# Performance work log

Measured on AMD Instinct MI355X. Metric: run time of the kernel, lower is better.

The kernel has to match this reference:

```python
import jax, jax.numpy as jnp
import numpy as np

NUM_ENTITIES = 100000
NUM_RELATIONS = 500
DIM = 256
NUM_TRIANGLES = 300000
NUM_TETRAS = 150000
ET_EDGES = 900000   # ~3 entities per triangle
TT_EDGES = 600000   # ~4 triangles per tetra
ENT_TET_EDGES = 600000
BATCH = 8192


def _mean_aggregate(src_idx, dst_idx, src, num_dst):
    """Scatter-mean of src[src_idx] into num_dst buckets keyed by dst_idx."""
    agg = jax.ops.segment_sum(src[src_idx], dst_idx, num_segments=num_dst)
    cnt = jax.ops.segment_sum(jnp.ones_like(dst_idx, dtype=src.dtype), dst_idx,
                              num_segments=num_dst)
    return agg / jnp.maximum(cnt, 1.0)[:, None]


def setup_inputs() -> dict:
    key = jax.random.key(0)
    ks = jax.random.split(key, 16)
    s = 1.0 / np.sqrt(DIM)
    E = jax.random.normal(ks[0], (NUM_ENTITIES, DIM), jnp.float32) * s
    R = jax.random.normal(ks[1], (NUM_RELATIONS, DIM), jnp.float32) * s
    lin2_w = jax.random.normal(ks[2], (DIM, DIM), jnp.float32) * s
    lin2_b = jnp.zeros((DIM,), jnp.float32)
    lin3_w = jax.random.normal(ks[3], (DIM, DIM), jnp.float32) * s
    lin3_b = jnp.zeros((DIM,), jnp.float32)
    t2e_w = jax.random.normal(ks[4], (DIM, DIM), jnp.float32) * s
    t2e_b = jnp.zeros((DIM,), jnp.float32)
    fusion_alpha = jnp.zeros((2,), jnp.float32)
    gamma = jnp.array([12.0], jnp.float32)
    # bipartite edge lists: row 0 = src indices, row 1 = dst indices
    et = jnp.stack([
        jax.random.randint(ks[5], (ET_EDGES,), 0, NUM_ENTITIES),
        jax.random.randint(ks[6], (ET_EDGES,), 0, NUM_TRIANGLES)], axis=0)
    tt = jnp.stack([
        jax.random.randint(ks[7], (TT_EDGES,), 0, NUM_TRIANGLES),
        jax.random.randint(ks[8], (TT_EDGES,), 0, NUM_TETRAS)], axis=0)
    # entity_tetra_index: row 0 = entity, row 1 = tetra (flipped inside model)
    etet = jnp.stack([
        jax.random.randint(ks[9], (ENT_TET_EDGES,), 0, NUM_ENTITIES),
        jax.random.randint(ks[10], (ENT_TET_EDGES,), 0, NUM_TETRAS)], axis=0)
    triples = jnp.stack([
        jax.random.randint(ks[11], (BATCH,), 0, NUM_ENTITIES),
        jax.random.randint(ks[12], (BATCH,), 0, NUM_RELATIONS),
        jax.random.randint(ks[13], (BATCH,), 0, NUM_ENTITIES)], axis=1)
    return {"E": E, "R": R, "lin2_w": lin2_w, "lin2_b": lin2_b,
            "lin3_w": lin3_w, "lin3_b": lin3_b, "t2e_w": t2e_w, "t2e_b": t2e_b,
            "fusion_alpha": fusion_alpha, "gamma": gamma,
            "entity_triangle_index": et, "triangle_tetra_index": tt,
            "entity_tetra_index": etet, "triples": triples,
            "num_triangles": NUM_TRIANGLES, "num_tetras": NUM_TETRAS}


def reference(E, R, lin2_w, lin2_b, lin3_w, lin3_b, t2e_w, t2e_b,
              fusion_alpha, gamma, entity_triangle_index, triangle_tetra_index,
              entity_tetra_index, triples, num_triangles, num_tetras):
    # gnn2: entity -> triangle (scatter-mean + Linear + ReLU)
    tri_agg = _mean_aggregate(entity_triangle_index[0], entity_triangle_index[1],
                              E, num_triangles)                      # [T, d]
    tri_emb = jax.nn.relu(tri_agg @ lin2_w.T + lin2_b)
    # gnn3: triangle -> tetra
    tet_agg = _mean_aggregate(triangle_tetra_index[0], triangle_tetra_index[1],
                              tri_emb, num_tetras)                   # [K, d]
    tet_emb = jax.nn.relu(tet_agg @ lin3_w.T + lin3_b)
    tet_proj = tet_emb @ t2e_w.T + t2e_b                             # [K, d]
    # tetra -> entity (edge index flipped: src=tetra, dst=entity)
    v_topo = _mean_aggregate(entity_tetra_index[1], entity_tetra_index[0],
                             tet_proj, E.shape[0])                   # [N, d]
    # learned fusion
    w = jax.nn.softmax(fusion_alpha)
    V = w[0] * E + w[1] * v_topo
    # TransE scoring: gamma - ||V[h] + R[r] - V[t]||
    h, r, t = triples[:, 0], triples[:, 1], triples[:, 2]
    diff = V[h] + R[r] - V[t]
    return gamma[0] - jnp.sqrt(jnp.sum(diff * diff, axis=-1))
```

## Files before the change

### kernel.cpp

```cpp
#include <hip/hip_runtime.h>
#include <hip/hip_bf16.h>
#include <math.h>

#define DIM 256
#define SBS 256
#define SIT 16
#define NT   300000
#define NTET 150000

typedef __attribute__((ext_vector_type(8))) short          bf16x8;
typedef __attribute__((ext_vector_type(8))) unsigned short u16x8;
typedef __attribute__((ext_vector_type(4))) float          f32x4;

__device__ inline float b2f(unsigned short u) {
    union { unsigned int i; float f; } c; c.i = ((unsigned int)u) << 16; return c.f;
}
__device__ inline unsigned short f2b(float f) {
    __hip_bfloat16 h = __float2bfloat16(f);
    return *reinterpret_cast<unsigned short*>(&h);
}
__device__ inline bool bmget(const unsigned* bm, int i) {
    return (bm[i >> 5] >> (i & 31)) & 1u;
}

__global__ __launch_bounds__(256) void k_cast3(
    const float* __restrict__ w2, const float* __restrict__ w3,
    const float* __restrict__ wt, unsigned short* __restrict__ out)
{
    int i = (blockIdx.x * 256 + threadIdx.x) * 4;
    const float* src; int l;
    if (i < 65536)       { src = w2; l = i; }
    else if (i < 131072) { src = w3; l = i - 65536; }
    else                 { src = wt; l = i - 131072; }
    float4 v = *(const float4*)(src + l);
    ushort4 o; o.x = f2b(v.x); o.y = f2b(v.y); o.z = f2b(v.z); o.w = f2b(v.w);
    *(ushort4*)(out + i) = o;
}

__global__ __launch_bounds__(256) void k_mark(
    const int* __restrict__ trip, unsigned* __restrict__ bm, int B)
{
    int i = blockIdx.x * 256 + threadIdx.x;
    if (i < 2 * B) {
        int ent = trip[(i >> 1) * 3 + ((i & 1) ? 2 : 0)];
        atomicOr(&bm[ent >> 5], 1u << (ent & 31));
    }
}

__global__ __launch_bounds__(256) void k_markf(
    const int* __restrict__ mi, const int* __restrict__ ci,
    const unsigned* __restrict__ bmIn, unsigned* __restrict__ bmOut, int n)
{
    int e = blockIdx.x * 256 + threadIdx.x;
    if (e < n && bmget(bmIn, ci[e])) {
        int m = mi[e];
        atomicOr(&bmOut[m >> 5], 1u << (m & 31));
    }
}

__global__ __launch_bounds__(256) void k_count_all(
    const int* __restrict__ et, const int* __restrict__ tt, const int* __restrict__ etet,
    const unsigned* __restrict__ bmTri, const unsigned* __restrict__ bmTet,
    const unsigned* __restrict__ bmEnt, int* __restrict__ cnt,
    int ET, int TT, int ETET)
{
    int e = blockIdx.x * 256 + threadIdx.x;
    if (e < ET) {
        int d = et[ET + e];
        if (bmget(bmTri, d)) atomicAdd(&cnt[d], 1);
    } else if (e < ET + TT) {
        int i = e - ET;
        int d = tt[TT + i];
        if (bmget(bmTet, d)) atomicAdd(&cnt[NT + d], 1);
    } else if (e < ET + TT + ETET) {
        int i = e - ET - TT;
        int d = etet[i];
        if (bmget(bmEnt, d)) atomicAdd(&cnt[NT + NTET + d], 1);
    }
}

__global__ __launch_bounds__(SBS) void k_scan_block(
    const int* __restrict__ cnt, int* __restrict__ rowOff,
    int* __restrict__ blockSums, int n)
{
    __shared__ int lds[SBS];
    const int t = threadIdx.x;
    const int tbase = blockIdx.x * SBS * SIT + t * SIT;
    int v[SIT]; int tsum = 0;
    #pragma unroll
    for (int i = 0; i < SIT; ++i) {
        int idx = tbase + i;
        v[i] = (idx < n) ? cnt[idx] : 0;
        tsum += v[i];
    }
    lds[t] = tsum;
    __syncthreads();
    #pragma unroll
    for (int off = 1; off < SBS; off <<= 1) {
        int y = (t >= off) ? lds[t - off] : 0;
        __syncthreads();
        lds[t] += y;
        __syncthreads();
    }
    int incl = lds[t];
    int run = incl - tsum;
    #pragma unroll
    for (int i = 0; i < SIT; ++i) {
        int idx = tbase + i;
        if (idx < n) rowOff[idx] = run;
        run += v[i];
    }
    if (t == SBS - 1) blockSums[blockIdx.x] = incl;
}

__global__ __launch_bounds__(SBS) void k_scan_sums(int* __restrict__ bs, int nb)
{
    __shared__ int lds[SBS];
    const int t = threadIdx.x;
    int v = (t < nb) ? bs[t] : 0;
    lds[t] = v;
    __syncthreads();
    #pragma unroll
    for (int off = 1; off < SBS; off <<= 1) {
        int y = (t >= off) ? lds[t - off] : 0;
        __syncthreads();
        lds[t] += y;
        __syncthreads();
    }
    if (t < nb) {
        bs[t] = lds[t] - v;
        if (t == nb - 1) bs[nb] = lds[t];
    }
}

__global__ __launch_bounds__(256) void k_scan_add(
    int* __restrict__ rowOff, int* __restrict__ cursor,
    const int* __restrict__ bs, int n, int nb)
{
    int i = blockIdx.x * 256 + threadIdx.x;
    if (i < n) {
        int v = rowOff[i] + bs[i / (SBS * SIT)];
        rowOff[i] = v;
        cursor[i] = v;
    }
    if (i == 0) rowOff[n] = bs[nb];
}

__global__ __launch_bounds__(256) void k_place_all(
    const int* __restrict__ et, const int* __restrict__ tt, const int* __restrict__ etet,
    const unsigned* __restrict__ bmTri, const unsigned* __restrict__ bmTet,
    const unsigned* __restrict__ bmEnt, int* __restrict__ cursor,
    int* __restrict__ sorted, int ET, int TT, int ETET)
{
    int e = blockIdx.x * 256 + threadIdx.x;
    if (e < ET) {
        int d = et[ET + e];
        if (bmget(bmTri, d)) sorted[atomicAdd(&cursor[d], 1)] = et[e];
    } else if (e < ET + TT) {
        int i = e - ET;
        int d = tt[TT + i];
        if (bmget(bmTet, d)) sorted[atomicAdd(&cursor[NT + d], 1)] = tt[i];
    } else if (e < ET + TT + ETET) {
        int i = e - ET - TT;
        int d = etet[i];
        if (bmget(bmEnt, d)) sorted[atomicAdd(&cursor[NT + NTET + d], 1)] = etet[ETET + i];
    }
}

template<int EPI>
__global__ __launch_bounds__(256) void k_gather(
    const unsigned short* __restrict__ src, const int* __restrict__ sorted,
    const int* __restrict__ rowOff, const float* __restrict__ bias,
    const float* __restrict__ E, const float* __restrict__ alpha,
    const unsigned* __restrict__ bm, void* __restrict__ out, int ndst)
{
    int d    = (blockIdx.x * 256 + threadIdx.x) >> 6;
    int lane = threadIdx.x & 63;
    if (d >= ndst) return;
    if (!bmget(bm, d)) return;
    int e0 = rowOff[d], e1 = rowOff[d + 1];
    float ax = 0.f, ay = 0.f, az = 0.f, aw = 0.f;
    int base = e0;
    for (; base + 4 <= e1; base += 4) {
        #pragma unroll
        for (int j = 0; j < 4; ++j) {
            int s = sorted[base + j];
            ushort4 u = *(const ushort4*)(src + (size_t)s * DIM + lane * 4);
            ax += b2f(u.x); ay += b2f(u.y); az += b2f(u.z); aw += b2f(u.w);
        }
    }
    if (base < e1) {
        #pragma unroll
        for (int j = 0; j < 4; ++j) {
            int ee = base + j;
            int ec = (ee < e1) ? ee : (e1 - 1);
            int s  = sorted[ec];
            ushort4 u = *(const ushort4*)(src + (size_t)s * DIM + lane * 4);
            float g = (ee < e1) ? 1.0f : 0.0f;
            ax += g * b2f(u.x); ay += g * b2f(u.y);
            az += g * b2f(u.z); aw += g * b2f(u.w);
        }
    }
    float inv = 1.0f / fmaxf((float)(e1 - e0), 1.0f);
    ax *= inv; ay *= inv; az *= inv; aw *= inv;
    if (EPI == 0) {
        float4 bv = *(const float4*)(bias + lane * 4);
        ax = fmaxf(ax + bv.x, 0.f); ay = fmaxf(ay + bv.y, 0.f);
        az = fmaxf(az + bv.z, 0.f); aw = fmaxf(aw + bv.w, 0.f);
        ushort4 o; o.x = f2b(ax); o.y = f2b(ay); o.z = f2b(az); o.w = f2b(aw);
        *(ushort4*)((unsigned short*)out + (size_t)d * DIM + lane * 4) = o;
    } else if (EPI == 1) {
        ushort4 o; o.x = f2b(ax); o.y = f2b(ay); o.z = f2b(az); o.w = f2b(aw);
        *(ushort4*)((unsigned short*)out + (size_t)d * DIM + lane * 4) = o;
    } else {
        float a0 = alpha[0], a1 = alpha[1];
        float mx = fmaxf(a0, a1);
        float x0 = expf(a0 - mx), x1 = expf(a1 - mx);
        float w0 = x0 / (x0 + x1), w1 = x1 / (x0 + x1);
        float4 ev = *(const float4*)(E + (size_t)d * DIM + lane * 4);
        float4 o;
        o.x = w0 * ev.x + w1 * ax; o.y = w0 * ev.y + w1 * ay;
        o.z = w0 * ev.z + w1 * az; o.w = w0 * ev.w + w1 * aw;
        *(float4*)((float*)out + (size_t)d * DIM + lane * 4) = o;
    }
}

template<bool AF32, bool RELU, bool BIAS>
__global__ __launch_bounds__(256) void k_gemm_mfma(
    const void* __restrict__ Ap, const unsigned short* __restrict__ Wb,
    const float* __restrict__ bias, unsigned short* __restrict__ Cp, int M)
{
    __shared__ unsigned short As[128 * 64];
    __shared__ unsigned short Ws[128 * 64];
    const int tid  = threadIdx.x;
    const int m0   = blockIdx.x * 128;
    const int n0   = blockIdx.y * 128;
    const int wid  = tid >> 6, lane = tid & 63;
    const int wr   = wid >> 1, wc = wid & 1;
    const int sp   = tid & 7;
    const int sr   = tid >> 3;
    const int fr   = lane & 15;
    const int fc   = lane >> 4;

    f32x4 acc[4][4] = {};
    for (int k0 = 0; k0 < DIM; k0 += 64) {
        __syncthreads();
        #pragma unroll
        for (int rr = 0; rr < 4; ++rr) {
            int row = sr + rr * 32;
            int gm  = m0 + row; if (gm >= M) gm = M - 1;
            unsigned off = row * 128 + ((sp * 16) ^ ((row & 7) << 4));
            if (AF32) {
                const float* g = (const float*)Ap + (size_t)gm * DIM + k0 + sp * 8;
                float4 lo = *(const float4*)g;
                float4 hi = *(const float4*)(g + 4);
                u16x8 v;
                v[0] = f2b(lo.x); v[1] = f2b(lo.y); v[2] = f2b(lo.z); v[3] = f2b(lo.w);
                v[4] = f2b(hi.x); v[5] = f2b(hi.y); v[6] = f2b(hi.z); v[7] = f2b(hi.w);
                *(u16x8*)((char*)As + off) = v;
            } else {
                const unsigned short* g = (const unsigned short*)Ap + (size_t)gm * DIM + k0 + sp * 8;
                *(u16x8*)((char*)As + off) = *(const u16x8*)g;
            }
            const unsigned short* gw = Wb + (size_t)(n0 + row) * DIM + k0 + sp * 8;
            *(u16x8*)((char*)Ws + off) = *(const u16x8*)gw;
        }
        __syncthreads();
        #pragma unroll
        for (int kk = 0; kk < 2; ++kk) {
            bf16x8 aF[4], bF[4];
            unsigned cb = kk * 64 + fc * 16;
            #pragma unroll
            for (int i = 0; i < 4; ++i) {
                int arow = wr * 64 + i * 16 + fr;
                aF[i] = *(const bf16x8*)((char*)As + arow * 128 + (cb ^ ((arow & 7) << 4)));
                int wrow = wc * 64 + i * 16 + fr;
                bF[i] = *(const bf16x8*)((char*)Ws + wrow * 128 + (cb ^ ((wrow & 7) << 4)));
            }
            #pragma unroll
            for (int i = 0; i < 4; ++i)
                #pragma unroll
                for (int j = 0; j < 4; ++j)
                    acc[i][j] = __builtin_amdgcn_mfma_f32_16x16x32_bf16(
                        aF[i], bF[j], acc[i][j], 0, 0, 0);
        }
    }
    const int cnb   = n0 + wc * 64 + fr;
    const int rbase = m0 + wr * 64 + fc * 4;
    #pragma unroll
    for (int j = 0; j < 4; ++j) {
        float bv = BIAS ? bias[cnb + j * 16] : 0.0f;
        #pragma unroll
        for (int i = 0; i < 4; ++i) {
            #pragma unroll
            for (int q = 0; q < 4; ++q) {
                int m = rbase + i * 16 + q;
                if (m < M) {
                    float v = acc[i][j][q] + bv;
                    if (RELU) v = fmaxf(v, 0.f);
                    Cp[(size_t)m * DIM + cnb + j * 16] = f2b(v);
                }
            }
        }
    }
}

__global__ __launch_bounds__(256) void k_score(
    const float* __restrict__ V, const float* __restrict__ R,
    const int* __restrict__ triples, const float* __restrict__ gamma,
    float* __restrict__ out, int B)
{
    int t    = (blockIdx.x * 256 + threadIdx.x) >> 6;
    int lane = threadIdx.x & 63;
    if (t >= B) return;
    int h  = triples[t * 3 + 0];
    int r  = triples[t * 3 + 1];
    int tl = triples[t * 3 + 2];
    float4 vh = *(const float4*)(V + (size_t)h  * DIM + lane * 4);
    float4 vr = *(const float4*)(R + (size_t)r  * DIM + lane * 4);
    float4 vt = *(const float4*)(V + (size_t)tl * DIM + lane * 4);
    float dx = vh.x + vr.x - vt.x;
    float dy = vh.y + vr.y - vt.y;
    float dz = vh.z + vr.z - vt.z;
    float dw = vh.w + vr.w - vt.w;
    float s = dx * dx + dy * dy + dz * dz + dw * dw;
    #pragma unroll
    for (int off = 32; off > 0; off >>= 1) s += __shfl_xor(s, off);
    if (lane == 0) out[t] = gamma[0] - sqrtf(s);
}

extern "C" void kernel_launch(void* const* d_in, const int* in_sizes, int n_in,
                              void* d_out, int out_size, void* d_ws, size_t ws_size,
                              hipStream_t stream)
{
    const float* E      = (const float*)d_in[0];
    const float* R      = (const float*)d_in[1];
    const float* lin2_w = (const float*)d_in[2];
    const float* lin2_b = (const float*)d_in[3];
    const float* lin3_w = (const float*)d_in[4];
    const float* lin3_b = (const float*)d_in[5];
    const float* t2e_w  = (const float*)d_in[6];
    const float* t2e_b  = (const float*)d_in[7];
    const float* alpha  = (const float*)d_in[8];
    const float* gamma  = (const float*)d_in[9];
    const int*   et     = (const int*)d_in[10];
    const int*   tt     = (const int*)d_in[11];
    const int*   etet   = (const int*)d_in[12];
    const int*   trip   = (const int*)d_in[13];

    const int NE   = in_sizes[0] / DIM;
    const int ET   = in_sizes[10] / 2;
    const int TT   = in_sizes[11] / 2;
    const int ETET = in_sizes[12] / 2;
    const int B    = in_sizes[13] / 3;
    const int NTOT = NT + NTET + NE;
    const int ETOT = ET + TT + ETET;

    char* ws = (char*)d_ws;
    const size_t P1  = (size_t)NE * DIM * 4;
    const size_t IDX = P1 + (size_t)NT * DIM * 2;
    unsigned short* EW      = (unsigned short*)ws;
    unsigned short* tetAgg  = (unsigned short*)ws;
    float*          V       = (float*)ws;
    unsigned short* triEmb  = (unsigned short*)(ws + P1);
    unsigned short* tetEmb  = (unsigned short*)(ws + P1);
    unsigned short* tetProj = (unsigned short*)(ws + P1) + (size_t)NTET * DIM;
    size_t off = IDX;
    int* sortedAll = (int*)(ws + off); off += (size_t)ETOT * 4;
    int* rowOffAll = (int*)(ws + off); off += ((size_t)(NTOT + 1) * 4 + 15) & ~15ull;
    int* cursorAll = (int*)(ws + off); off += (size_t)NTOT * 4;
    int* blockSums = (int*)(ws + off); off += 1040;
    unsigned short* Wb = (unsigned short*)(ws + off); off += 3 * 131072;
    char* zbase = ws + off;
    int*      cntAll = (int*)(ws + off);      off += (size_t)NTOT * 4;
    unsigned* bmEnt  = (unsigned*)(ws + off); off += ((size_t)(NE   + 31) / 32) * 4;
    unsigned* bmTet  = (unsigned*)(ws + off); off += ((size_t)(NTET + 31) / 32) * 4;
    unsigned* bmTri  = (unsigned*)(ws + off); off += ((size_t)(NT   + 31) / 32) * 4;
    size_t zsize = (size_t)(ws + off - zbase);
    if (ws_size < off) return;

    unsigned short* W2b = Wb;
    unsigned short* W3b = Wb + 65536;
    unsigned short* Wtb = Wb + 131072;

    hipMemsetAsync(zbase, 0, zsize, stream);
    k_cast3<<<192, 256, 0, stream>>>(lin2_w, lin3_w, t2e_w, Wb);
    dim3 gE((NE + 127) / 128, 2);
    k_gemm_mfma<true, false, false><<<gE, 256, 0, stream>>>(E, W2b, nullptr, EW, NE);

    k_mark<<<(2 * B + 255) / 256, 256, 0, stream>>>(trip, bmEnt, B);
    k_markf<<<(ETET + 255) / 256, 256, 0, stream>>>(etet + ETET, etet, bmEnt, bmTet, ETET);
    k_markf<<<(TT + 255) / 256, 256, 0, stream>>>(tt, tt + TT, bmTet, bmTri, TT);

    k_count_all<<<(ETOT + 255) / 256, 256, 0, stream>>>(
        et, tt, etet, bmTri, bmTet, bmEnt, cntAll, ET, TT, ETET);
    int nb = (NTOT + SBS * SIT - 1) / (SBS * SIT);
    k_scan_block<<<nb, SBS, 0, stream>>>(cntAll, rowOffAll, blockSums, NTOT);
    k_scan_sums<<<1, SBS, 0, stream>>>(blockSums, nb);
    k_scan_add<<<(NTOT + 255) / 256, 256, 0, stream>>>(rowOffAll, cursorAll,
                                                       blockSums, NTOT, nb);
    k_place_all<<<(ETOT + 255) / 256, 256, 0, stream>>>(
        et, tt, etet, bmTri, bmTet, bmEnt, cursorAll, sortedAll, ET, TT, ETET);

    k_gather<0><<<(NT + 3) / 4, 256, 0, stream>>>(EW, sortedAll, rowOffAll, lin2_b,
                                                  nullptr, nullptr, bmTri, triEmb, NT);

    k_gather<1><<<(NTET + 3) / 4, 256, 0, stream>>>(triEmb, sortedAll, rowOffAll + NT,
                                                    nullptr, nullptr, nullptr, bmTet,
                                                    tetAgg, NTET);
    dim3 gT((NTET + 127) / 128, 2);
    k_gemm_mfma<false, true, true><<<gT, 256, 0, stream>>>(tetAgg, W3b, lin3_b, tetEmb, NTET);
    k_gemm_mfma<false, false, true><<<gT, 256, 0, stream>>>(tetEmb, Wtb, t2e_b, tetProj, NTET);

    k_gather<2><<<(NE + 3) / 4, 256, 0, stream>>>(tetProj, sortedAll,
                                                  rowOffAll + NT + NTET, nullptr,
                                                  E, alpha, bmEnt, V, NE);

    k_score<<<(B + 3) / 4, 256, 0, stream>>>(V, R, trip, gamma, (float*)d_out, B);
}
```

Baseline: 479.2 us.

## Compact needed tetras for GEMMs, half-wave gather rows, skip redundant atomicOr

Needed tetrahedra are compacted through a prefix scan over the tetra bitmap, and the two tetra GEMMs then run only over the compacted row count, with blocks beyond it exiting early. Each gather writes into or reads from the compacted rows through this index. The gather kernel now handles two destinations per wavefront, using 16-byte loads per half-wave, which improves load width and occupancy for sparse masks. It also checks a bit before calling atomicOr, trading a plain read for fewer atomics.

Result: faster. 410.4 us (-14.4%).

```diff
diff --git a/kernel.cpp b/kernel.cpp
--- a/kernel.cpp
+++ b/kernel.cpp
@@ -54,8 +54,16 @@
     int e = blockIdx.x * 256 + threadIdx.x;
     if (e < n && bmget(bmIn, ci[e])) {
         int m = mi[e];
-        atomicOr(&bmOut[m >> 5], 1u << (m & 31));
-    }
+        unsigned msk = 1u << (m & 31);
+        if (!(bmOut[m >> 5] & msk)) atomicOr(&bmOut[m >> 5], msk);
+    }
+}
+
+__global__ __launch_bounds__(256) void k_bits(
+    const unsigned* __restrict__ bm, int* __restrict__ out, int n)
+{
+    int i = blockIdx.x * 256 + threadIdx.x;
+    if (i < n) out[i] = (bm[i >> 5] >> (i & 31)) & 1u;
 }
 
 __global__ __launch_bounds__(256) void k_count_all(
@@ -135,13 +143,13 @@
 
 __global__ __launch_bounds__(256) void k_scan_add(
     int* __restrict__ rowOff, int* __restrict__ cursor,
-    const int* __restrict__ bs, int n, int nb)
+    const int* __restrict__ bs, int n, int nb, int ncur)
 {
     int i = blockIdx.x * 256 + threadIdx.x;
     if (i < n) {
         int v = rowOff[i] + bs[i / (SBS * SIT)];
         rowOff[i] = v;
-        cursor[i] = v;
+        if (i < ncur) cursor[i] = v;
     }
     if (i == 0) rowOff[n] = bs[nb];
 }
@@ -172,68 +180,92 @@
     const unsigned short* __restrict__ src, const int* __restrict__ sorted,
     const int* __restrict__ rowOff, const float* __restrict__ bias,
     const float* __restrict__ E, const float* __restrict__ alpha,
-    const unsigned* __restrict__ bm, void* __restrict__ out, int ndst)
-{
-    int d    = (blockIdx.x * 256 + threadIdx.x) >> 6;
-    int lane = threadIdx.x & 63;
-    if (d >= ndst) return;
-    if (!bmget(bm, d)) return;
-    int e0 = rowOff[d], e1 = rowOff[d + 1];
-    float ax = 0.f, ay = 0.f, az = 0.f, aw = 0.f;
-    int base = e0;
-    for (; base + 4 <= e1; base += 4) {
+    const unsigned* __restrict__ bm, const int* __restrict__ cmpOff,
+    void* __restrict__ out, int ndst)
+{
+    const int g    = (blockIdx.x * 256 + threadIdx.x) >> 6;
+    const int lane = threadIdx.x & 63;
+    const int half = lane >> 5;
+    const int hl   = lane & 31;
+    const int d    = g * 2 + half;
+    const bool need = (d < ndst) && bmget(bm, d);
+    if (!__any(need)) return;
+    const int cmpBase = (EPI >= 1) ? cmpOff[0] : 0;
+    int e0 = 0, e1 = 0;
+    if (need) { e0 = rowOff[d]; e1 = rowOff[d + 1]; }
+    float acc[8] = {0.f, 0.f, 0.f, 0.f, 0.f, 0.f, 0.f, 0.f};
+    for (int p = e0; p < e1; p += 4) {
+        u16x8 u[4]; float gt[4];
         #pragma unroll
         for (int j = 0; j < 4; ++j) {
-            int s = sorted[base + j];
-            ushort4 u = *(const ushort4*)(src + (size_t)s * DIM + lane * 4);
-            ax += b2f(u.x); ay += b2f(u.y); az += b2f(u.z); aw += b2f(u.w);
-        }
-    }
-    if (base < e1) {
-        #pragma unroll
-        for (int j = 0; j < 4; ++j) {
-            int ee = base + j;
+            int ee = p + j;
             int ec = (ee < e1) ? ee : (e1 - 1);
             int s  = sorted[ec];
-            ushort4 u = *(const ushort4*)(src + (size_t)s * DIM + lane * 4);
-            float g = (ee < e1) ? 1.0f : 0.0f;
-            ax += g * b2f(u.x); ay += g * b2f(u.y);
-            az += g * b2f(u.z); aw += g * b2f(u.w);
-        }
+            if (EPI == 2) s = cmpOff[s] - cmpBase;
+            u[j]  = *(const u16x8*)(src + (size_t)s * DIM + hl * 8);
+            gt[j] = (ee < e1) ? 1.0f : 0.0f;
+        }
+        #pragma unroll
+        for (int j = 0; j < 4; ++j)
+            #pragma unroll
+            for (int k = 0; k < 8; ++k)
+                acc[k] += gt[j] * b2f(u[j][k]);
     }
     float inv = 1.0f / fmaxf((float)(e1 - e0), 1.0f);
-    ax *= inv; ay *= inv; az *= inv; aw *= inv;
+    #pragma unroll
+    for (int k = 0; k < 8; ++k) acc[k] *= inv;
     if (EPI == 0) {
-        float4 bv = *(const float4*)(bias + lane * 4);
-        ax = fmaxf(ax + bv.x, 0.f); ay = fmaxf(ay + bv.y, 0.f);
-        az = fmaxf(az + bv.z, 0.f); aw = fmaxf(aw + bv.w, 0.f);
-        ushort4 o; o.x = f2b(ax); o.y = f2b(ay); o.z = f2b(az); o.w = f2b(aw);
-        *(ushort4*)((unsigned short*)out + (size_t)d * DIM + lane * 4) = o;
+        float4 bl = *(const float4*)(bias + hl * 8);
+        float4 bh = *(const float4*)(bias + hl * 8 + 4);
+        float bb[8] = {bl.x, bl.y, bl.z, bl.w, bh.x, bh.y, bh.z, bh.w};
+        if (need) {
+            u16x8 o;
+            #pragma unroll
+            for (int k = 0; k < 8; ++k) o[k] = f2b(fmaxf(acc[k] + bb[k], 0.f));
+            *(u16x8*)((unsigned short*)out + (size_t)d * DIM + hl * 8) = o;
+        }
     } else if (EPI == 1) {
-        ushort4 o; o.x = f2b(ax); o.y = f2b(ay); o.z = f2b(az); o.w = f2b(aw);
-        *(ushort4*)((unsigned short*)out + (size_t)d * DIM + lane * 4) = o;
+        if (need) {
+            int cd = cmpOff[d] - cmpBase;
+            u16x8 o;
+            #pragma unroll
+            for (int k = 0; k < 8; ++k) o[k] = f2b(acc[k]);
+            *(u16x8*)((unsigned short*)out + (size_t)cd * DIM + hl * 8) = o;
+        }
     } else {
-        float a0 = alpha[0], a1 = alpha[1];
-        float mx = fmaxf(a0, a1);
-        float x0 = expf(a0 - mx), x1 = expf(a1 - mx);
+        float a0 = alpha[0], a1v = alpha[1];
+        float mx = fmaxf(a0, a1v);
+        float x0 = expf(a0 - mx), x1 = expf(a1v - mx);
         float w0 = x0 / (x0 + x1), w1 = x1 / (x0 + x1);
-        float4 ev = *(const float4*)(E + (size_t)d * DIM + lane * 4);
-        float4 o;
-        o.x = w0 * ev.x + w1 * ax; o.y = w0 * ev.y + w1 * ay;
-        o.z = w0 * ev.z + w1 * az; o.w = w0 * ev.w + w1 * aw;
-        *(float4*)((float*)out + (size_t)d * DIM + lane * 4) = o;
-    }
-}
-
-template<bool AF32, bool RELU, bool BIAS>
+        if (need) {
+            const float* er = E + (size_t)d * DIM + hl * 8;
+            float4 el = *(const float4*)er;
+            float4 eh = *(const float4*)(er + 4);
+            float4 o0, o1;
+            o0.x = w0 * el.x + w1 * acc[0]; o0.y = w0 * el.y + w1 * acc[1];
+            o0.z = w0 * el.z + w1 * acc[2]; o0.w = w0 * el.w + w1 * acc[3];
+            o1.x = w0 * eh.x + w1 * acc[4]; o1.y = w0 * eh.y + w1 * acc[5];
+            o1.z = w0 * eh.z + w1 * acc[6]; o1.w = w0 * eh.w + w1 * acc[7];
+            float* orow = (float*)out + (size_t)d * DIM + hl * 8;
+            *(float4*)orow = o0;
+            *(float4*)(orow + 4) = o1;
+        }
+    }
+}
+
+template<bool AF32, bool RELU, bool BIAS, bool DYNM>
 __global__ __launch_bounds__(256) void k_gemm_mfma(
     const void* __restrict__ Ap, const unsigned short* __restrict__ Wb,
-    const float* __restrict__ bias, unsigned short* __restrict__ Cp, int M)
-{
+    const float* __restrict__ bias, unsigned short* __restrict__ Cp,
+    int Ms, const int* __restrict__ cmpOff)
+{
+    int M = Ms;
+    if (DYNM) M = cmpOff[NTET] - cmpOff[0];
+    const int m0 = blockIdx.x * 128;
+    if (m0 >= M) return;
     __shared__ unsigned short As[128 * 64];
     __shared__ unsigned short Ws[128 * 64];
     const int tid  = threadIdx.x;
-    const int m0   = blockIdx.x * 128;
     const int n0   = blockIdx.y * 128;
     const int wid  = tid >> 6, lane = tid & 63;
     const int wr   = wid >> 1, wc = wid & 1;
@@ -348,13 +380,14 @@
     const int*   etet   = (const int*)d_in[12];
     const int*   trip   = (const int*)d_in[13];
 
-    const int NE   = in_sizes[0] / DIM;
-    const int ET   = in_sizes[10] / 2;
-    const int TT   = in_sizes[11] / 2;
-    const int ETET = in_sizes[12] / 2;
-    const int B    = in_sizes[13] / 3;
-    const int NTOT = NT + NTET + NE;
-    const int ETOT = ET + TT + ETET;
+    const int NE    = in_sizes[0] / DIM;
+    const int ET    = in_sizes[10] / 2;
+    const int TT    = in_sizes[11] / 2;
+    const int ETET  = in_sizes[12] / 2;
+    const int B     = in_sizes[13] / 3;
+    const int NTOT  = NT + NTET + NE;
+    const int NTOT2 = NTOT + NTET;
+    const int ETOT  = ET + TT + ETET;
 
     char* ws = (char*)d_ws;
     const size_t P1  = (size_t)NE * DIM * 4;
@@ -367,12 +400,12 @@
     unsigned short* tetProj = (unsigned short*)(ws + P1) + (size_t)NTET * DIM;
     size_t off = IDX;
     int* sortedAll = (int*)(ws + off); off += (size_t)ETOT * 4;
-    int* rowOffAll = (int*)(ws + off); off += ((size_t)(NTOT + 1) * 4 + 15) & ~15ull;
+    int* rowOffAll = (int*)(ws + off); off += ((size_t)(NTOT2 + 1) * 4 + 15) & ~15ull;
     int* cursorAll = (int*)(ws + off); off += (size_t)NTOT * 4;
     int* blockSums = (int*)(ws + off); off += 1040;
     unsigned short* Wb = (unsigned short*)(ws + off); off += 3 * 131072;
     char* zbase = ws + off;
-    int*      cntAll = (int*)(ws + off);      off += (size_t)NTOT * 4;
+    int*      cntAll = (int*)(ws + off);      off += (size_t)NTOT2 * 4;
     unsigned* bmEnt  = (unsigned*)(ws + off); off += ((size_t)(NE   + 31) / 32) * 4;
     unsigned* bmTet  = (unsigned*)(ws + off); off += ((size_t)(NTET + 31) / 32) * 4;
     unsigned* bmTri  = (unsigned*)(ws + off); off += ((size_t)(NT   + 31) / 32) * 4;
@@ -382,39 +415,45 @@
     unsigned short* W2b = Wb;
     unsigned short* W3b = Wb + 65536;
     unsigned short* Wtb = Wb + 131072;
+    int* cmpOff = rowOffAll + NTOT;
 
     hipMemsetAsync(zbase, 0, zsize, stream);
     k_cast3<<<192, 256, 0, stream>>>(lin2_w, lin3_w, t2e_w, Wb);
     dim3 gE((NE + 127) / 128, 2);
-    k_gemm_mfma<true, false, false><<<gE, 256, 0, stream>>>(E, W2b, nullptr, EW, NE);
+    k_gemm_mfma<true, false, false, false><<<gE, 256, 0, stream>>>(
+        E, W2b, nullptr, EW, NE, nullptr);
 
     k_mark<<<(2 * B + 255) / 256, 256, 0, stream>>>(trip, bmEnt, B);
     k_markf<<<(ETET + 255) / 256, 256, 0, stream>>>(etet + ETET, etet, bmEnt, bmTet, ETET);
     k_markf<<<(TT + 255) / 256, 256, 0, stream>>>(tt, tt + TT, bmTet, bmTri, TT);
+    k_bits<<<(NTET + 255) / 256, 256, 0, stream>>>(bmTet, cntAll + NTOT, NTET);
 
     k_count_all<<<(ETOT + 255) / 256, 256, 0, stream>>>(
         et, tt, etet, bmTri, bmTet, bmEnt, cntAll, ET, TT, ETET);
-    int nb = (NTOT + SBS * SIT - 1) / (SBS * SIT);
-    k_scan_block<<<nb, SBS, 0, stream>>>(cntAll, rowOffAll, blockSums, NTOT);
+    int nb = (NTOT2 + SBS * SIT - 1) / (SBS * SIT);
+    k_scan_block<<<nb, SBS, 0, stream>>>(cntAll, rowOffAll, blockSums, NTOT2);
     k_scan_sums<<<1, SBS, 0, stream>>>(blockSums, nb);
-    k_scan_add<<<(NTOT + 255) / 256, 256, 0, stream>>>(rowOffAll, cursorAll,
-                                                       blockSums, NTOT, nb);
+    k_scan_add<<<(NTOT2 + 255) / 256, 256, 0, stream>>>(rowOffAll, cursorAll,
+                                                        blockSums, NTOT2, nb, NTOT);
     k_place_all<<<(ETOT + 255) / 256, 256, 0, stream>>>(
         et, tt, etet, bmTri, bmTet, bmEnt, cursorAll, sortedAll, ET, TT, ETET);
 
-    k_gather<0><<<(NT + 3) / 4, 256, 0, stream>>>(EW, sortedAll, rowOffAll, lin2_b,
-                                                  nullptr, nullptr, bmTri, triEmb, NT);
-
-    k_gather<1><<<(NTET + 3) / 4, 256, 0, stream>>>(triEmb, sortedAll, rowOffAll + NT,
+    k_gather<0><<<(NT + 7) / 8, 256, 0, stream>>>(EW, sortedAll, rowOffAll, lin2_b,
+                                                  nullptr, nullptr, bmTri, cmpOff,
+                                                  triEmb, NT);
+
+    k_gather<1><<<(NTET + 7) / 8, 256, 0, stream>>>(triEmb, sortedAll, rowOffAll + NT,
                                                     nullptr, nullptr, nullptr, bmTet,
-                                                    tetAgg, NTET);
+                                                    cmpOff, tetAgg, NTET);
     dim3 gT((NTET + 127) / 128, 2);
-    k_gemm_mfma<false, true, true><<<gT, 256, 0, stream>>>(tetAgg, W3b, lin3_b, tetEmb, NTET);
-    k_gemm_mfma<false, false, true><<<gT, 256, 0, stream>>>(tetEmb, Wtb, t2e_b, tetProj, NTET);
-
-    k_gather<2><<<(NE + 3) / 4, 256, 0, stream>>>(tetProj, sortedAll,
+    k_gemm_mfma<false, true, true, true><<<gT, 256, 0, stream>>>(
+        tetAgg, W3b, lin3_b, tetEmb, NTET, cmpOff);
+    k_gemm_mfma<false, false, true, true><<<gT, 256, 0, stream>>>(
+        tetEmb, Wtb, t2e_b, tetProj, NTET, cmpOff);
+
+    k_gather<2><<<(NE + 7) / 8, 256, 0, stream>>>(tetProj, sortedAll,
                                                   rowOffAll + NT + NTET, nullptr,
-                                                  E, alpha, bmEnt, V, NE);
+                                                  E, alpha, bmEnt, cmpOff, V, NE);
 
     k_score<<<(B + 3) / 4, 256, 0, stream>>>(V, R, trip, gamma, (float*)d_out, B);
 }
```
